# Kernel optimization log

Hardware: AMD Instinct MI355X
Metric: run time of the kernel (lower is better)

The kernel has to match this reference:

```python
import jax, jax.numpy as jnp
import numpy as np

B, A, L, D, IN = 4096, 11, 8, 256, 4
HID = 64  # mlp_dim in MS_HGNN modules
LINE = 64  # line_embedding output dim


def setup_inputs() -> dict:
    key = jax.random.key(0)
    ks = jax.random.split(key, 17)
    s = 0.02
    f = jnp.float32
    return {
        "inputs": jax.random.normal(ks[0], (B * A, L, IN), f),
        "W_in": jax.random.normal(ks[1], (IN, D), f) * s,
        "b_in": jnp.zeros((D,), f),
        "W_pos": jax.random.normal(ks[2], (2 * D, D), f) * s,
        "b_pos": jnp.zeros((D,), f),
        "W_fc2": jax.random.normal(ks[3], (L * D, D), f) * s,
        "b_fc2": jnp.zeros((D,), f),
        "W_fc3": jax.random.normal(ks[4], (D + A, D), f) * s,
        "b_fc3": jnp.zeros((D,), f),
        "Wh1": jax.random.normal(ks[5], (D, HID), f) * s,
        "We1": jax.random.normal(ks[6], (2 * HID, HID), f) * s,
        "Wn1": jax.random.normal(ks[7], (HID, D), f) * s,
        "Wh2": jax.random.normal(ks[8], (D, HID), f) * s,
        "We2": jax.random.normal(ks[9], (2 * HID, HID), f) * s,
        "Wn2": jax.random.normal(ks[10], (HID, D), f) * s,
        "W_line": jax.random.normal(ks[11], (D, LINE), f) * s,
        "batch_size": B,
        "agent_num": A,
    }


def _nmp(xf, Wh, We, Wn, w=None):
    # one round of neural message passing over the (hyper)graph of agents
    h = jax.nn.relu(xf @ Wh)  # [B, A, HID]
    b, a, hd = h.shape
    hi = jnp.broadcast_to(h[:, :, None, :], (b, a, a, hd))
    hj = jnp.broadcast_to(h[:, None, :, :], (b, a, a, hd))
    e = jax.nn.relu(jnp.concatenate([hi, hj], -1) @ We)  # [B, A, A, HID]
    if w is None:
        agg = e.mean(axis=2)
    else:
        agg = (w[..., None] * e).sum(axis=2) / (w.sum(axis=2)[..., None] + 1e-6)
    return agg @ Wn  # [B, A, D]


def reference(inputs, W_in, b_in, W_pos, b_pos, W_fc2, b_fc2, W_fc3, b_fc3,
              Wh1, We1, Wn1, Wh2, We2, Wn2, W_line, batch_size, agent_num):
    d = W_in.shape[1]
    length = inputs.shape[1]
    # input_fc
    tf_in = inputs @ W_in + b_in  # [B*A, L, D]
    # positional encoding (sin/cos interleaved), concat + fc (dropout in eval)
    pos = jnp.arange(length, dtype=tf_in.dtype)[:, None]
    div = jnp.exp(jnp.arange(0, d, 2, dtype=tf_in.dtype) * (-np.log(10000.0) / d))
    ang = pos * div  # [L, D/2]
    pe = jnp.stack([jnp.sin(ang), jnp.cos(ang)], -1).reshape(length, d)
    x = jnp.concatenate([tf_in, jnp.broadcast_to(pe, tf_in.shape)], -1) @ W_pos + b_pos
    # flatten time, input_fc2
    x = x.reshape(batch_size, agent_num, length * d)
    ftraj = x @ W_fc2 + b_fc2  # [B, A, D]
    # add_category (identity one-hot per agent) + input_fc3
    eye = jnp.broadcast_to(jnp.eye(agent_num, dtype=ftraj.dtype),
                           (batch_size, agent_num, agent_num))
    ftraj = jnp.concatenate([ftraj, eye], -1) @ W_fc3 + b_fc3
    # cosine-similarity correlation + per-scene adaptive thresholding
    q = ftraj / jnp.linalg.norm(ftraj, axis=2, keepdims=True)
    corr = jnp.einsum('bad,bcd->bac', q, q)
    a = corr.min(axis=(1, 2), keepdims=True)
    thr = jnp.where(a < 0.4, 0.4,
                    jnp.where((a > 0.4) & (a < 0.6), a + 0.1, a + 0.03))
    corr = jnp.where(corr < thr, jnp.zeros_like(corr), corr)
    adj = (corr > 0).astype(ftraj.dtype)  # binarized dynamic grouping mask
    # ordinary fully-connected interaction
    ftraj_inter = _nmp(ftraj, Wh1, We1, Wn1)
    # group-masked hyper interaction + line embedding
    hyp = _nmp(ftraj, Wh2, We2, Wn2, adj)
    feat_one = hyp @ W_line  # [B, A, LINE]
    out = jnp.concatenate([ftraj, ftraj_inter, feat_one], -1)
    return out.reshape(batch_size * agent_num, -1)
```

## Files before the change

kernel.cpp:

```cpp
#include <hip/hip_runtime.h>

#define TPB 256
#define TPM 192

constexpr int B_ = 4096, A_ = 11;
constexpr int R_ = B_ * A_;

constexpr int M_O     = 0;
constexpr int M2_O    = 8192;
constexpr int WC_O    = 16384;
constexpr int XB_O    = 19712;
constexpr int CB_O    = 21760;
constexpr int B2_O    = 22016;
constexpr int WN2L_O  = 24832;
constexpr int MH1_O   = 28928;
constexpr int BH1_O   = 30976;
constexpr int MH2_O   = 16384;
constexpr int BH2_O   = 18432;


__global__ __launch_bounds__(TPB) void k_preAB(const float* __restrict__ Win,
                                               const float* __restrict__ bin,
                                               const float* __restrict__ Wpos,
                                               const float* __restrict__ bpos,
                                               const float* __restrict__ Wn2,
                                               const float* __restrict__ Wline,
                                               float* __restrict__ ws) {
    __shared__ float red[8 * 33];
    const int t = threadIdx.x, o8 = t & 31, ks = t >> 5;
    const int bx = blockIdx.x;
    if (bx < 32) {
        int o = bx * 32 + o8, i = o >> 8, j = o & 255;
        const float* Ar = Win + i * 256;
        float p = 0.f;
        #pragma unroll 8
        for (int d = ks * 32; d < ks * 32 + 32; ++d) p += Ar[d] * Wpos[d * 256 + j];
        red[ks * 33 + o8] = p;
        __syncthreads();
        if (t < 32) {
            float s = 0.f;
            #pragma unroll
            for (int m = 0; m < 8; ++m) s += red[m * 33 + t];
            ws[WC_O + bx * 32 + t] = s;
        }
    } else if (bx < 96) {
        int o = (bx - 32) * 32 + o8, l = o >> 8, j = o & 255;
        const float c0 = -logf(10000.f) / 256.f;
        float p = 0.f;
        for (int d = ks * 64; d < ks * 64 + 64; ++d) {
            float a;
            if (d < 256) a = bin[d];
            else {
                int dd = d - 256;
                float freq = expf((float)(dd & ~1) * c0);
                float ang = (float)l * freq;
                a = (dd & 1) ? cosf(ang) : sinf(ang);
            }
            p += a * Wpos[d * 256 + j];
        }
        red[ks * 33 + o8] = p;
        __syncthreads();
        if (t < 32) {
            int oo = (bx - 32) * 32 + t;
            float s = bpos[oo & 255];
            #pragma unroll
            for (int m = 0; m < 8; ++m) s += red[m * 33 + t];
            ws[XB_O + oo] = s;
        }
    } else {
        int o = (bx - 96) * 32 + o8, k = o >> 6, c = o & 63;
        const float* Ar = Wn2 + k * 256;
        float p = 0.f;
        #pragma unroll 8
        for (int d = ks * 32; d < ks * 32 + 32; ++d) p += Ar[d] * Wline[d * 64 + c];
        red[ks * 33 + o8] = p;
        __syncthreads();
        if (t < 32) {
            float s = 0.f;
            #pragma unroll
            for (int m = 0; m < 8; ++m) s += red[m * 33 + t];
            ws[WN2L_O + (bx - 96) * 32 + t] = s;
        }
    }
}

__global__ __launch_bounds__(TPB) void k_preC(const float* __restrict__ Wfc2,
                                              const float* __restrict__ bfc2,
                                              float* __restrict__ ws) {
    __shared__ float red[8 * 33];
    const int t = threadIdx.x, o8 = t & 31, ks = t >> 5;
    const int bx = blockIdx.x;
    if (bx < 256) {
        int o = bx * 32 + o8, k = o >> 8, j = o & 255;
        int l = k >> 2, i = k & 3;
        const float* Ar = ws + WC_O + i * 256;
        const float* Br = Wfc2 + l * 65536 + j;
        float p = 0.f;
        #pragma unroll 8
        for (int d = ks * 32; d < ks * 32 + 32; ++d) p += Ar[d] * Br[d * 256];
        red[ks * 33 + o8] = p;
        __syncthreads();
        if (t < 32) {
            float s = 0.f;
            #pragma unroll
            for (int m = 0; m < 8; ++m) s += red[m * 33 + t];
            ws[M_O + bx * 32 + t] = s;
        }
    } else {
        int j = (bx - 256) * 32 + o8;
        const float* Ar = ws + XB_O;
        float p = 0.f;
        #pragma unroll 4
        for (int dk = ks * 256; dk < ks * 256 + 256; ++dk) p += Ar[dk] * Wfc2[dk * 256 + j];
        red[ks * 33 + o8] = p;
        __syncthreads();
        if (t < 32) {
            int jj = (bx - 256) * 32 + t;
            float s = bfc2[jj];
            #pragma unroll
            for (int m = 0; m < 8; ++m) s += red[m * 33 + t];
            ws[CB_O + jj] = s;
        }
    }
}

__global__ __launch_bounds__(TPB) void k_preD(const float* __restrict__ Wfc3,
                                              const float* __restrict__ bfc3,
                                              float* __restrict__ ws) {
    __shared__ float red[8 * 33];
    const int t = threadIdx.x, o8 = t & 31, ks = t >> 5;
    const int bx = blockIdx.x;
    if (bx < 256) {
        int o = bx * 32 + o8, k = o >> 8, j = o & 255;
        const float* Ar = ws + M_O + k * 256;
        float p = 0.f;
        #pragma unroll 8
        for (int d = ks * 32; d < ks * 32 + 32; ++d) p += Ar[d] * Wfc3[d * 256 + j];
        red[ks * 33 + o8] = p;
        __syncthreads();
        if (t < 32) {
            float s = 0.f;
            #pragma unroll
            for (int m = 0; m < 8; ++m) s += red[m * 33 + t];
            ws[M2_O + bx * 32 + t] = s;
        }
    } else {
        int o = (bx - 256) * 32 + o8, j = o & 255;
        const float* Ar = ws + CB_O;
        float p = 0.f;
        #pragma unroll 8
        for (int d = ks * 32; d < ks * 32 + 32; ++d) p += Ar[d] * Wfc3[d * 256 + j];
        red[ks * 33 + o8] = p;
        __syncthreads();
        if (t < 32) {
            int oo = (bx - 256) * 32 + t;
            int aa = oo >> 8, jj = oo & 255;
            float s = bfc3[jj] + Wfc3[(256 + aa) * 256 + jj];
            #pragma unroll
            for (int m = 0; m < 8; ++m) s += red[m * 33 + t];
            ws[B2_O + oo] = s;
        }
    }
}

__global__ __launch_bounds__(TPB) void k_preE(const float* __restrict__ Wh1,
                                              const float* __restrict__ Wh2,
                                              float* __restrict__ ws) {
    __shared__ float red[8 * 33];
    const int t = threadIdx.x, o8 = t & 31, ks = t >> 5;
    const int bx = blockIdx.x;
    const float* Bw;  int oo_base;  int out_o;  int mode;
    if (bx < 64)       { mode = 0; out_o = MH1_O; oo_base = bx * 32;         Bw = Wh1; }
    else if (bx < 86)  { mode = 1; out_o = BH1_O; oo_base = (bx - 64) * 32;  Bw = Wh1; }
    else if (bx < 150) { mode = 0; out_o = MH2_O; oo_base = (bx - 86) * 32;  Bw = Wh2; }
    else               { mode = 1; out_o = BH2_O; oo_base = (bx - 150) * 32; Bw = Wh2; }
    int o = oo_base + o8;
    int r = o >> 6, c = o & 63;
    const float* Aw = ws + (mode == 0 ? M2_O : B2_O) + r * 256;
    float p = 0.f;
    #pragma unroll 8
    for (int d = ks * 32; d < ks * 32 + 32; ++d) p += Aw[d] * Bw[d * 64 + c];
    red[ks * 33 + o8] = p;
    __syncthreads();
    if (t < 32) {
        float s = 0.f;
        #pragma unroll
        for (int m = 0; m < 8; ++m) s += red[m * 33 + t];
        ws[out_o + oo_base + t] = s;
    }
}


__global__ __launch_bounds__(TPM) void k_main(const float* __restrict__ in,
                                              const float* __restrict__ We1g,
                                              const float* __restrict__ We2g,
                                              const float* __restrict__ Wn1,
                                              const float* __restrict__ ws,
                                              float* out) {
    __shared__ float inS[44 * 36];
    __shared__ float bufA[44 * 68];
    __shared__ float bufB[44 * 68];
    __shared__ float Bs[2048];
    __shared__ float dcS[484];
    __shared__ float thrS[4];
    const int t = threadIdx.x;
    const int rg = t >> 4, cg = t & 15;
    const int r0 = rg * 4, c0 = cg * 4;
    const int rowBlk = blockIdx.x * 44;
    const bool act = rg < 11;

    float4 pf0, pf1, pf2;
    auto pfLoad = [&](const float4* lo, const float4* hi) {
        pf0 = lo[t];
        pf1 = (t < 64) ? lo[t + 192] : hi[t - 64];
        if (t < 128) pf2 = hi[t + 128];
    };
    auto pfStore = [&]() {
        float4* d = (float4*)Bs;
        d[t] = pf0; d[t + 192] = pf1;
        if (t < 128) d[t + 384] = pf2;
    };

    pfLoad((const float4*)(ws + M2_O), (const float4*)(ws + M2_O) + 256);
    for (int o = t; o < 352; o += TPM) {
        int row = o >> 3, c4 = o & 7;
        *(float4*)&inS[row * 36 + c4 * 4] =
            *(const float4*)&in[(size_t)(rowBlk + row) * 32 + c4 * 4];
    }
    __syncthreads();

    float acc[4][16];
    #pragma unroll
    for (int r = 0; r < 4; ++r)
        #pragma unroll
        for (int c = 0; c < 16; ++c) acc[r][c] = 0.f;
    for (int kh = 0; kh < 4; ++kh) {
        pfStore();
        if (kh < 3) pfLoad((const float4*)(ws + M2_O) + (kh + 1) * 512,
                           (const float4*)(ws + M2_O) + (kh + 1) * 512 + 256);
        else        pfLoad((const float4*)(ws + MH1_O), (const float4*)(ws + MH1_O) + 256);
        __syncthreads();
        if (act) {
            #pragma unroll
            for (int kq = 0; kq < 2; ++kq) {
                float av[4][4];
                #pragma unroll
                for (int r = 0; r < 4; ++r) {
                    float4 a4 = *(const float4*)&inS[(r0 + r) * 36 + kh * 8 + kq * 4];
                    av[r][0] = a4.x; av[r][1] = a4.y; av[r][2] = a4.z; av[r][3] = a4.w;
                }
                #pragma unroll
                for (int kk = 0; kk < 4; ++kk) {
                    float4 b[4];
                    #pragma unroll
                    for (int j = 0; j < 4; ++j)
                        b[j] = *(const float4*)&Bs[(kq * 4 + kk) * 256 + c0 + j * 64];
                    #pragma unroll
                    for (int r = 0; r < 4; ++r) {
                        float a = av[r][kk];
                        #pragma unroll
                        for (int j = 0; j < 4; ++j) {
                            acc[r][j * 4 + 0] += a * b[j].x;
                            acc[r][j * 4 + 1] += a * b[j].y;
                            acc[r][j * 4 + 2] += a * b[j].z;
                            acc[r][j * 4 + 3] += a * b[j].w;
                        }
                    }
                }
            }
        }
        __syncthreads();
    }
    if (act) {
        #pragma unroll
        for (int r = 0; r < 4; ++r) {
            int row = r0 + r, il = row % 11;
            size_t ob = (size_t)(rowBlk + row) * 576;
            #pragma unroll
            for (int j = 0; j < 4; ++j) {
                float4 b2 = *(const float4*)&ws[B2_O + il * 256 + c0 + j * 64];
                acc[r][j * 4 + 0] += b2.x; acc[r][j * 4 + 1] += b2.y;
                acc[r][j * 4 + 2] += b2.z; acc[r][j * 4 + 3] += b2.w;
                *(float4*)&out[ob + c0 + j * 64] =
                    make_float4(acc[r][j * 4 + 0], acc[r][j * 4 + 1],
                                acc[r][j * 4 + 2], acc[r][j * 4 + 3]);
            }
        }
    }

    bool has0 = false, has1 = false;
    int s0_ = 0, i0_ = 0, j0_ = 0, s1_ = 0, i1_ = 0, j1_ = 0;
    {
        int idx = t;
        if (idx < 264) {
            has0 = true; s0_ = idx / 66; int p = idx % 66; int i = 0;
            while (p >= 11 - i) { p -= 11 - i; ++i; }
            i0_ = i; j0_ = i + p;
        }
        idx = t + TPM;
        if (idx < 264) {
            has1 = true; s1_ = idx / 66; int p = idx % 66; int i = 0;
            while (p >= 11 - i) { p -= 11 - i; ++i; }
            i1_ = i; j1_ = i + p;
        }
    }
    float dacc0 = 0.f, dacc1 = 0.f;
    for (int sl = 0; sl < 4; ++sl) {
        if (act) {
            #pragma unroll
            for (int r = 0; r < 4; ++r)
                *(float4*)&bufA[(r0 + r) * 68 + c0] =
                    make_float4(acc[r][sl * 4 + 0], acc[r][sl * 4 + 1],
                                acc[r][sl * 4 + 2], acc[r][sl * 4 + 3]);
        }
        __syncthreads();
        if (has0) {
            const float* ra = &bufA[(s0_ * 11 + i0_) * 68];
            const float* rb = &bufA[(s0_ * 11 + j0_) * 68];
            #pragma unroll
            for (int c = 0; c < 16; ++c) {
                float4 a = *(const float4*)&ra[c * 4];
                float4 b = *(const float4*)&rb[c * 4];
                dacc0 += a.x * b.x + a.y * b.y + a.z * b.z + a.w * b.w;
            }
        }
        if (has1) {
            const float* ra = &bufA[(s1_ * 11 + i1_) * 68];
            const float* rb = &bufA[(s1_ * 11 + j1_) * 68];
            #pragma unroll
            for (int c = 0; c < 16; ++c) {
                float4 a = *(const float4*)&ra[c * 4];
                float4 b = *(const float4*)&rb[c * 4];
                dacc1 += a.x * b.x + a.y * b.y + a.z * b.z + a.w * b.w;
            }
        }
        __syncthreads();
    }
    if (has0) { dcS[s0_ * 121 + i0_ * 11 + j0_] = dacc0;
                dcS[s0_ * 121 + j0_ * 11 + i0_] = dacc0; }
    if (has1) { dcS[s1_ * 121 + i1_ * 11 + j1_] = dacc1;
                dcS[s1_ * 121 + j1_ * 11 + i1_] = dacc1; }
    __syncthreads();

    {
        float cc0, cc1, cc2 = 0.f;
        {
            int idx = t; int si = idx / 121, p = idx % 121, i = p / 11, j = p % 11;
            cc0 = dcS[idx] * rsqrtf(dcS[si * 121 + i * 12] * dcS[si * 121 + j * 12]);
        }
        {
            int idx = t + TPM; int si = idx / 121, p = idx % 121, i = p / 11, j = p % 11;
            cc1 = dcS[idx] * rsqrtf(dcS[si * 121 + i * 12] * dcS[si * 121 + j * 12]);
        }
        if (t + 2 * TPM < 484) {
            int idx = t + 2 * TPM; int si = idx / 121, p = idx % 121, i = p / 11, j = p % 11;
            cc2 = dcS[idx] * rsqrtf(dcS[si * 121 + i * 12] * dcS[si * 121 + j * 12]);
        }
        __syncthreads();
        dcS[t] = cc0;
        dcS[t + TPM] = cc1;
        if (t + 2 * TPM < 484) dcS[t + 2 * TPM] = cc2;
    }
    __syncthreads();
    if (t < 4) {
        float mn = 3.0e38f;
        for (int p = 0; p < 121; ++p) mn = fminf(mn, dcS[t * 121 + p]);
        thrS[t] = (mn < 0.4f) ? 0.4f : ((mn > 0.4f && mn < 0.6f) ? mn + 0.1f : mn + 0.03f);
    }
    __syncthreads();

    float a1v[4][4];
    for (int st = 0; st < 2; ++st) {
        const float* bh = ws + (st ? BH2_O : BH1_O);
        const float* We = st ? We2g : We1g;
        float* hbuf = st ? bufB : bufA;
        pfStore();
        pfLoad((const float4*)(We), (const float4*)(We + 4096));
        __syncthreads();
        float hh[4][4];
        #pragma unroll
        for (int r = 0; r < 4; ++r)
            #pragma unroll
            for (int c = 0; c < 4; ++c) hh[r][c] = 0.f;
        if (act) {
            #pragma unroll
            for (int kq = 0; kq < 8; ++kq) {
                float av[4][4];
                #pragma unroll
                for (int r = 0; r < 4; ++r) {
                    float4 a4 = *(const float4*)&inS[(r0 + r) * 36 + kq * 4];
                    av[r][0] = a4.x; av[r][1] = a4.y; av[r][2] = a4.z; av[r][3] = a4.w;
                }
                #pragma unroll
                for (int kk = 0; kk < 4; ++kk) {
                    float4 b = *(const float4*)&Bs[(kq * 4 + kk) * 64 + c0];
                    #pragma unroll
                    for (int r = 0; r < 4; ++r) {
                        float a = av[r][kk];
                        hh[r][0] += a * b.x; hh[r][1] += a * b.y;
                        hh[r][2] += a * b.z; hh[r][3] += a * b.w;
                    }
                }
            }
            #pragma unroll
            for (int r = 0; r < 4; ++r) {
                int il = (r0 + r) % 11;
                float4 b = *(const float4*)&bh[il * 64 + c0];
                *(float4*)&hbuf[(r0 + r) * 68 + c0] =
                    make_float4(fmaxf(hh[r][0] + b.x, 0.f), fmaxf(hh[r][1] + b.y, 0.f),
                                fmaxf(hh[r][2] + b.z, 0.f), fmaxf(hh[r][3] + b.w, 0.f));
            }
        }
        __syncthreads();
        float uu[4][4], vv[4][4];
        #pragma unroll
        for (int r = 0; r < 4; ++r)
            #pragma unroll
            for (int c = 0; c < 4; ++c) { uu[r][c] = 0.f; vv[r][c] = 0.f; }
        for (int kh = 0; kh < 4; ++kh) {
            pfStore();
            if (kh < 3)
                pfLoad((const float4*)(We + (kh + 1) * 1024),
                       (const float4*)(We + 4096 + (kh + 1) * 1024));
            else if (st == 0)
                pfLoad((const float4*)(ws + MH2_O), (const float4*)(ws + MH2_O) + 256);
            else
                pfLoad((const float4*)(Wn1), (const float4*)(Wn1) + 256);
            __syncthreads();
            if (act) {
                #pragma unroll
                for (int kq = 0; kq < 4; ++kq) {
                    float av[4][4];
                    #pragma unroll
                    for (int r = 0; r < 4; ++r) {
                        float4 a4 = *(const float4*)&hbuf[(r0 + r) * 68 + kh * 16 + kq * 4];
                        av[r][0] = a4.x; av[r][1] = a4.y; av[r][2] = a4.z; av[r][3] = a4.w;
                    }
                    #pragma unroll
                    for (int kk = 0; kk < 4; ++kk) {
                        float4 bu = *(const float4*)&Bs[(kq * 4 + kk) * 64 + c0];
                        float4 bv = *(const float4*)&Bs[1024 + (kq * 4 + kk) * 64 + c0];
                        #pragma unroll
                        for (int r = 0; r < 4; ++r) {
                            float a = av[r][kk];
                            uu[r][0] += a * bu.x; uu[r][1] += a * bu.y;
                            uu[r][2] += a * bu.z; uu[r][3] += a * bu.w;
                            vv[r][0] += a * bv.x; vv[r][1] += a * bv.y;
                            vv[r][2] += a * bv.z; vv[r][3] += a * bv.w;
                        }
                    }
                }
            }
            __syncthreads();
        }
        if (act) {
            #pragma unroll
            for (int r = 0; r < 4; ++r)
                *(float4*)&bufB[(r0 + r) * 68 + c0] =
                    make_float4(vv[r][0], vv[r][1], vv[r][2], vv[r][3]);
        }
        __syncthreads();
        if (act) {
            #pragma unroll
            for (int r = 0; r < 4; ++r) {
                int row = r0 + r, s = row / 11, il = row - s * 11;
                float th = thrS[s];
                float t0 = 0.f, t1 = 0.f, t2 = 0.f, t3 = 0.f, cnt = 0.f;
                #pragma unroll
                for (int j = 0; j < 11; ++j) {
                    float4 vj = *(const float4*)&bufB[(s * 11 + j) * 68 + c0];
                    if (st == 0) {
                        t0 += fmaxf(uu[r][0] + vj.x, 0.f);
                        t1 += fmaxf(uu[r][1] + vj.y, 0.f);
                        t2 += fmaxf(uu[r][2] + vj.z, 0.f);
                        t3 += fmaxf(uu[r][3] + vj.w, 0.f);
                    } else {
                        float adj = (dcS[s * 121 + il * 11 + j] >= th) ? 1.f : 0.f;
                        t0 += adj * fmaxf(uu[r][0] + vj.x, 0.f);
                        t1 += adj * fmaxf(uu[r][1] + vj.y, 0.f);
                        t2 += adj * fmaxf(uu[r][2] + vj.z, 0.f);
                        t3 += adj * fmaxf(uu[r][3] + vj.w, 0.f);
                        cnt += adj;
                    }
                }
                float inv = (st == 0) ? (1.f / 11.f) : (1.f / (cnt + 1e-6f));
                a1v[r][0] = t0 * inv; a1v[r][1] = t1 * inv;
                a1v[r][2] = t2 * inv; a1v[r][3] = t3 * inv;
            }
        }
        __syncthreads();
        if (act) {
            float* dst = st ? bufB : bufA;
            #pragma unroll
            for (int r = 0; r < 4; ++r)
                *(float4*)&dst[(r0 + r) * 68 + c0] =
                    make_float4(a1v[r][0], a1v[r][1], a1v[r][2], a1v[r][3]);
        }
        __syncthreads();
    }

    {
        float ac2[4][16];
        #pragma unroll
        for (int r = 0; r < 4; ++r)
            #pragma unroll
            for (int c = 0; c < 16; ++c) ac2[r][c] = 0.f;
        for (int kh = 0; kh < 8; ++kh) {
            pfStore();
            if (kh < 7) pfLoad((const float4*)(Wn1) + (kh + 1) * 512,
                               (const float4*)(Wn1) + (kh + 1) * 512 + 256);
            else        pfLoad((const float4*)(ws + WN2L_O), (const float4*)(ws + WN2L_O) + 256);
            __syncthreads();
            if (act) {
                #pragma unroll
                for (int kq = 0; kq < 2; ++kq) {
                    float av[4][4];
                    #pragma unroll
                    for (int r = 0; r < 4; ++r) {
                        float4 a4 = *(const float4*)&bufA[(r0 + r) * 68 + kh * 8 + kq * 4];
                        av[r][0] = a4.x; av[r][1] = a4.y; av[r][2] = a4.z; av[r][3] = a4.w;
                    }
                    #pragma unroll
                    for (int kk = 0; kk < 4; ++kk) {
                        float4 b[4];
                        #pragma unroll
                        for (int j = 0; j < 4; ++j)
                            b[j] = *(const float4*)&Bs[(kq * 4 + kk) * 256 + c0 + j * 64];
                        #pragma unroll
                        for (int r = 0; r < 4; ++r) {
                            float a = av[r][kk];
                            #pragma unroll
                            for (int j = 0; j < 4; ++j) {
                                ac2[r][j * 4 + 0] += a * b[j].x;
                                ac2[r][j * 4 + 1] += a * b[j].y;
                                ac2[r][j * 4 + 2] += a * b[j].z;
                                ac2[r][j * 4 + 3] += a * b[j].w;
                            }
                        }
                    }
                }
            }
            __syncthreads();
        }
        if (act) {
            #pragma unroll
            for (int r = 0; r < 4; ++r) {
                size_t ob = (size_t)(rowBlk + r0 + r) * 576 + 256;
                #pragma unroll
                for (int j = 0; j < 4; ++j)
                    *(float4*)&out[ob + c0 + j * 64] =
                        make_float4(ac2[r][j * 4 + 0], ac2[r][j * 4 + 1],
                                    ac2[r][j * 4 + 2], ac2[r][j * 4 + 3]);
            }
        }
    }

    {
        float fa[4][4];
        #pragma unroll
        for (int r = 0; r < 4; ++r)
            #pragma unroll
            for (int c = 0; c < 4; ++c) fa[r][c] = 0.f;
        for (int kh = 0; kh < 2; ++kh) {
            pfStore();
            if (kh == 0) pfLoad((const float4*)(ws + WN2L_O) + 512,
                                (const float4*)(ws + WN2L_O) + 768);
            __syncthreads();
            if (act) {
                #pragma unroll
                for (int kq = 0; kq < 8; ++kq) {
                    float av[4][4];
                    #pragma unroll
                    for (int r = 0; r < 4; ++r) {
                        float4 a4 = *(const float4*)&bufB[(r0 + r) * 68 + kh * 32 + kq * 4];
                        av[r][0] = a4.x; av[r][1] = a4.y; av[r][2] = a4.z; av[r][3] = a4.w;
                    }
                    #pragma unroll
                    for (int kk = 0; kk < 4; ++kk) {
                        float4 b = *(const float4*)&Bs[(kq * 4 + kk) * 64 + c0];
                        #pragma unroll
                        for (int r = 0; r < 4; ++r) {
                            float a = av[r][kk];
                            fa[r][0] += a * b.x; fa[r][1] += a * b.y;
                            fa[r][2] += a * b.z; fa[r][3] += a * b.w;
                        }
                    }
                }
            }
            __syncthreads();
        }
        if (act) {
            #pragma unroll
            for (int r = 0; r < 4; ++r)
                *(float4*)&out[(size_t)(rowBlk + r0 + r) * 576 + 512 + c0] =
                    make_float4(fa[r][0], fa[r][1], fa[r][2], fa[r][3]);
        }
    }
}

extern "C" void kernel_launch(void* const* d_in, const int* in_sizes, int n_in,
                              void* d_out, int out_size, void* d_ws, size_t ws_size,
                              hipStream_t stream) {
    (void)in_sizes; (void)n_in; (void)out_size; (void)ws_size;
    const float* in     = (const float*)d_in[0];
    const float* W_in   = (const float*)d_in[1];
    const float* b_in   = (const float*)d_in[2];
    const float* W_pos  = (const float*)d_in[3];
    const float* b_pos  = (const float*)d_in[4];
    const float* W_fc2  = (const float*)d_in[5];
    const float* b_fc2  = (const float*)d_in[6];
    const float* W_fc3  = (const float*)d_in[7];
    const float* b_fc3  = (const float*)d_in[8];
    const float* Wh1    = (const float*)d_in[9];
    const float* We1    = (const float*)d_in[10];
    const float* Wn1    = (const float*)d_in[11];
    const float* Wh2    = (const float*)d_in[12];
    const float* We2    = (const float*)d_in[13];
    const float* Wn2    = (const float*)d_in[14];
    const float* W_line = (const float*)d_in[15];
    float* out = (float*)d_out;
    float* ws  = (float*)d_ws;

    k_preAB<<<224, TPB, 0, stream>>>(W_in, b_in, W_pos, b_pos, Wn2, W_line, ws);
    k_preC<<<264, TPB, 0, stream>>>(W_fc2, b_fc2, ws);
    k_preD<<<344, TPB, 0, stream>>>(W_fc3, b_fc3, ws);
    k_preE<<<172, TPB, 0, stream>>>(Wh1, Wh2, ws);
    k_main<<<1024, TPM, 0, stream>>>(in, We1, We2, Wn1, ws, out);
}
```

Before: 168.1 us.

## Split final Wn1/Wline projections into separate tail kernel and merge weight-prep kernels

```diff
diff --git a/kernel.cpp b/kernel.cpp
--- a/kernel.cpp
+++ b/kernel.cpp
@@ -9,44 +9,45 @@
 constexpr int M_O     = 0;
 constexpr int M2_O    = 8192;
 constexpr int WC_O    = 16384;
-constexpr int XB_O    = 19712;
-constexpr int CB_O    = 21760;
-constexpr int B2_O    = 22016;
-constexpr int WN2L_O  = 24832;
-constexpr int MH1_O   = 28928;
-constexpr int BH1_O   = 30976;
-constexpr int MH2_O   = 16384;
-constexpr int BH2_O   = 18432;
-
-
-__global__ __launch_bounds__(TPB) void k_preAB(const float* __restrict__ Win,
-                                               const float* __restrict__ bin,
-                                               const float* __restrict__ Wpos,
-                                               const float* __restrict__ bpos,
-                                               const float* __restrict__ Wn2,
-                                               const float* __restrict__ Wline,
-                                               float* __restrict__ ws) {
+constexpr int XB_O    = 17408;
+constexpr int CB_O    = 19456;
+constexpr int B2_O    = 19712;
+constexpr int WN2L_O  = 22528;
+constexpr int MH1_O   = 26624;
+constexpr int BH1_O   = 28672;
+constexpr int MH2_O   = 29376;
+constexpr int BH2_O   = 31424;
+constexpr int WFA1_O  = 32768;
+constexpr int WFA2_O  = 49152;
+constexpr int BEYE1_O = 65536;
+constexpr int BEYE2_O = 66240;
+constexpr int BB1_O   = 66944;
+constexpr int BB2_O   = 67008;
+constexpr int AG1_O   = 67584;
+constexpr int SZ_RH   = R_ * 64;
+constexpr int AG2_O   = AG1_O + SZ_RH;
+
+
+__global__ __launch_bounds__(TPB) void k_preA(const float* __restrict__ Win,
+                                              const float* __restrict__ bin,
+                                              const float* __restrict__ Wpos,
+                                              const float* __restrict__ bpos,
+                                              const float* __restrict__ Wn2,
+                                              const float* __restrict__ Wline,
+                                              const float* __restrict__ Wfc3,
+                                              const float* __restrict__ bfc3,
+                                              const float* __restrict__ Wh1,
+                                              const float* __restrict__ Wh2,
+                                              float* __restrict__ ws) {
     __shared__ float red[8 * 33];
     const int t = threadIdx.x, o8 = t & 31, ks = t >> 5;
     const int bx = blockIdx.x;
-    if (bx < 32) {
-        int o = bx * 32 + o8, i = o >> 8, j = o & 255;
-        const float* Ar = Win + i * 256;
-        float p = 0.f;
-        #pragma unroll 8
-        for (int d = ks * 32; d < ks * 32 + 32; ++d) p += Ar[d] * Wpos[d * 256 + j];
-        red[ks * 33 + o8] = p;
-        __syncthreads();
-        if (t < 32) {
-            float s = 0.f;
-            #pragma unroll
-            for (int m = 0; m < 8; ++m) s += red[m * 33 + t];
-            ws[WC_O + bx * 32 + t] = s;
-        }
-    } else if (bx < 96) {
-        int o = (bx - 32) * 32 + o8, l = o >> 8, j = o & 255;
+    float p = 0.f;
+    float base_add = 0.f;
+    int out_idx = -1;
+    if (bx < 64) {
+        int o = bx * 32 + o8, l = o >> 8, j = o & 255;
         const float c0 = -logf(10000.f) / 256.f;
-        float p = 0.f;
         for (int d = ks * 64; d < ks * 64 + 64; ++d) {
             float a;
             if (d < 256) a = bin[d];
@@ -58,29 +59,57 @@
             }
             p += a * Wpos[d * 256 + j];
         }
-        red[ks * 33 + o8] = p;
-        __syncthreads();
-        if (t < 32) {
-            int oo = (bx - 32) * 32 + t;
-            float s = bpos[oo & 255];
-            #pragma unroll
-            for (int m = 0; m < 8; ++m) s += red[m * 33 + t];
-            ws[XB_O + oo] = s;
-        }
+        out_idx = XB_O + o; base_add = bpos[j];
+    } else if (bx < 192) {
+        int o = (bx - 64) * 32 + o8, k = o >> 6, c = o & 63;
+        #pragma unroll 8
+        for (int d = ks * 32; d < ks * 32 + 32; ++d) p += Wn2[k * 256 + d] * Wline[d * 64 + c];
+        out_idx = WN2L_O + o;
+    } else if (bx < 704) {
+        int o = (bx - 192) * 32 + o8, e = o >> 6, c = o & 63;
+        #pragma unroll 8
+        for (int d = ks * 32; d < ks * 32 + 32; ++d) p += Wfc3[e * 256 + d] * Wh1[d * 64 + c];
+        out_idx = WFA1_O + o;
+    } else if (bx < 1216) {
+        int o = (bx - 704) * 32 + o8, e = o >> 6, c = o & 63;
+        #pragma unroll 8
+        for (int d = ks * 32; d < ks * 32 + 32; ++d) p += Wfc3[e * 256 + d] * Wh2[d * 64 + c];
+        out_idx = WFA2_O + o;
+    } else if (bx < 1238) {
+        int o = (bx - 1216) * 32 + o8, a = o >> 6, c = o & 63;
+        #pragma unroll 8
+        for (int d = ks * 32; d < ks * 32 + 32; ++d) p += Wfc3[(256 + a) * 256 + d] * Wh1[d * 64 + c];
+        out_idx = BEYE1_O + o;
+    } else if (bx < 1260) {
+        int o = (bx - 1238) * 32 + o8, a = o >> 6, c = o & 63;
+        #pragma unroll 8
+        for (int d = ks * 32; d < ks * 32 + 32; ++d) p += Wfc3[(256 + a) * 256 + d] * Wh2[d * 64 + c];
+        out_idx = BEYE2_O + o;
+    } else if (bx < 1262) {
+        int c = (bx - 1260) * 32 + o8;
+        #pragma unroll 8
+        for (int d = ks * 32; d < ks * 32 + 32; ++d) p += bfc3[d] * Wh1[d * 64 + c];
+        out_idx = BB1_O + c;
+    } else if (bx < 1264) {
+        int c = (bx - 1262) * 32 + o8;
+        #pragma unroll 8
+        for (int d = ks * 32; d < ks * 32 + 32; ++d) p += bfc3[d] * Wh2[d * 64 + c];
+        out_idx = BB2_O + c;
     } else {
-        int o = (bx - 96) * 32 + o8, k = o >> 6, c = o & 63;
-        const float* Ar = Wn2 + k * 256;
-        float p = 0.f;
-        #pragma unroll 8
-        for (int d = ks * 32; d < ks * 32 + 32; ++d) p += Ar[d] * Wline[d * 64 + c];
-        red[ks * 33 + o8] = p;
-        __syncthreads();
-        if (t < 32) {
-            float s = 0.f;
-            #pragma unroll
-            for (int m = 0; m < 8; ++m) s += red[m * 33 + t];
-            ws[WN2L_O + (bx - 96) * 32 + t] = s;
-        }
+        int o = (bx - 1264) * 32 + o8, i = o >> 8, j = o & 255;
+        #pragma unroll 8
+        for (int d = ks * 32; d < ks * 32 + 32; ++d) p += Win[i * 256 + d] * Wpos[d * 256 + j];
+        out_idx = WC_O + o;
+    }
+    red[ks * 33 + o8] = p;
+    __shared__ float baseS[32];
+    if (ks == 0) baseS[o8] = base_add;
+    __syncthreads();
+    if (t < 32) {
+        float s = baseS[t];
+        #pragma unroll
+        for (int m = 0; m < 8; ++m) s += red[m * 33 + t];
+        ws[out_idx - o8 + t] = s;
     }
 }
 
@@ -130,76 +159,81 @@
     __shared__ float red[8 * 33];
     const int t = threadIdx.x, o8 = t & 31, ks = t >> 5;
     const int bx = blockIdx.x;
+    float p = 0.f;
+    int out_base = -1;
+    float fin = 0.f;
+    int oo32 = 0;
     if (bx < 256) {
         int o = bx * 32 + o8, k = o >> 8, j = o & 255;
         const float* Ar = ws + M_O + k * 256;
-        float p = 0.f;
         #pragma unroll 8
         for (int d = ks * 32; d < ks * 32 + 32; ++d) p += Ar[d] * Wfc3[d * 256 + j];
-        red[ks * 33 + o8] = p;
-        __syncthreads();
-        if (t < 32) {
-            float s = 0.f;
-            #pragma unroll
-            for (int m = 0; m < 8; ++m) s += red[m * 33 + t];
-            ws[M2_O + bx * 32 + t] = s;
-        }
-    } else {
+        out_base = M2_O; oo32 = bx * 32;
+    } else if (bx < 344) {
         int o = (bx - 256) * 32 + o8, j = o & 255;
         const float* Ar = ws + CB_O;
-        float p = 0.f;
         #pragma unroll 8
         for (int d = ks * 32; d < ks * 32 + 32; ++d) p += Ar[d] * Wfc3[d * 256 + j];
-        red[ks * 33 + o8] = p;
-        __syncthreads();
-        if (t < 32) {
-            int oo = (bx - 256) * 32 + t;
+        out_base = B2_O; oo32 = (bx - 256) * 32;
+    } else if (bx < 408) {
+        int o = (bx - 344) * 32 + o8, k = o >> 6, c = o & 63;
+        const float* Ar = ws + M_O + k * 256;
+        const float* Br = ws + WFA1_O;
+        #pragma unroll 8
+        for (int d = ks * 32; d < ks * 32 + 32; ++d) p += Ar[d] * Br[d * 64 + c];
+        out_base = MH1_O; oo32 = (bx - 344) * 32;
+    } else if (bx < 472) {
+        int o = (bx - 408) * 32 + o8, k = o >> 6, c = o & 63;
+        const float* Ar = ws + M_O + k * 256;
+        const float* Br = ws + WFA2_O;
+        #pragma unroll 8
+        for (int d = ks * 32; d < ks * 32 + 32; ++d) p += Ar[d] * Br[d * 64 + c];
+        out_base = MH2_O; oo32 = (bx - 408) * 32;
+    } else if (bx < 494) {
+        int o = (bx - 472) * 32 + o8, c = o & 63;
+        const float* Ar = ws + CB_O;
+        const float* Br = ws + WFA1_O;
+        #pragma unroll 8
+        for (int d = ks * 32; d < ks * 32 + 32; ++d) p += Ar[d] * Br[d * 64 + c];
+        out_base = BH1_O; oo32 = (bx - 472) * 32;
+    } else {
+        int o = (bx - 494) * 32 + o8, c = o & 63;
+        const float* Ar = ws + CB_O;
+        const float* Br = ws + WFA2_O;
+        #pragma unroll 8
+        for (int d = ks * 32; d < ks * 32 + 32; ++d) p += Ar[d] * Br[d * 64 + c];
+        out_base = BH2_O; oo32 = (bx - 494) * 32;
+    }
+    red[ks * 33 + o8] = p;
+    __syncthreads();
+    if (t < 32) {
+        int oo = oo32 + t;
+        float s;
+        if (out_base == B2_O) {
             int aa = oo >> 8, jj = oo & 255;
-            float s = bfc3[jj] + Wfc3[(256 + aa) * 256 + jj];
-            #pragma unroll
-            for (int m = 0; m < 8; ++m) s += red[m * 33 + t];
-            ws[B2_O + oo] = s;
-        }
-    }
-}
-
-__global__ __launch_bounds__(TPB) void k_preE(const float* __restrict__ Wh1,
-                                              const float* __restrict__ Wh2,
-                                              float* __restrict__ ws) {
-    __shared__ float red[8 * 33];
-    const int t = threadIdx.x, o8 = t & 31, ks = t >> 5;
-    const int bx = blockIdx.x;
-    const float* Bw;  int oo_base;  int out_o;  int mode;
-    if (bx < 64)       { mode = 0; out_o = MH1_O; oo_base = bx * 32;         Bw = Wh1; }
-    else if (bx < 86)  { mode = 1; out_o = BH1_O; oo_base = (bx - 64) * 32;  Bw = Wh1; }
-    else if (bx < 150) { mode = 0; out_o = MH2_O; oo_base = (bx - 86) * 32;  Bw = Wh2; }
-    else               { mode = 1; out_o = BH2_O; oo_base = (bx - 150) * 32; Bw = Wh2; }
-    int o = oo_base + o8;
-    int r = o >> 6, c = o & 63;
-    const float* Aw = ws + (mode == 0 ? M2_O : B2_O) + r * 256;
-    float p = 0.f;
-    #pragma unroll 8
-    for (int d = ks * 32; d < ks * 32 + 32; ++d) p += Aw[d] * Bw[d * 64 + c];
-    red[ks * 33 + o8] = p;
-    __syncthreads();
-    if (t < 32) {
-        float s = 0.f;
+            s = bfc3[jj] + Wfc3[(256 + aa) * 256 + jj];
+        } else if (out_base == BH1_O) {
+            int aa = oo >> 6, cc = oo & 63;
+            s = ws[BB1_O + cc] + ws[BEYE1_O + aa * 64 + cc];
+        } else if (out_base == BH2_O) {
+            int aa = oo >> 6, cc = oo & 63;
+            s = ws[BB2_O + cc] + ws[BEYE2_O + aa * 64 + cc];
+        } else s = 0.f;
         #pragma unroll
         for (int m = 0; m < 8; ++m) s += red[m * 33 + t];
-        ws[out_o + oo_base + t] = s;
-    }
+        ws[out_base + oo] = s;
+    }
+    (void)fin;
 }
 
 
 __global__ __launch_bounds__(TPM) void k_main(const float* __restrict__ in,
                                               const float* __restrict__ We1g,
                                               const float* __restrict__ We2g,
-                                              const float* __restrict__ Wn1,
-                                              const float* __restrict__ ws,
+                                              float* ws,
                                               float* out) {
     __shared__ float inS[44 * 36];
-    __shared__ float bufA[44 * 68];
-    __shared__ float bufB[44 * 68];
+    __shared__ float buf[44 * 68];
     __shared__ float Bs[2048];
     __shared__ float dcS[484];
     __shared__ float thrS[4];
@@ -309,14 +343,14 @@
         if (act) {
             #pragma unroll
             for (int r = 0; r < 4; ++r)
-                *(float4*)&bufA[(r0 + r) * 68 + c0] =
+                *(float4*)&buf[(r0 + r) * 68 + c0] =
                     make_float4(acc[r][sl * 4 + 0], acc[r][sl * 4 + 1],
                                 acc[r][sl * 4 + 2], acc[r][sl * 4 + 3]);
         }
         __syncthreads();
         if (has0) {
-            const float* ra = &bufA[(s0_ * 11 + i0_) * 68];
-            const float* rb = &bufA[(s0_ * 11 + j0_) * 68];
+            const float* ra = &buf[(s0_ * 11 + i0_) * 68];
+            const float* rb = &buf[(s0_ * 11 + j0_) * 68];
             #pragma unroll
             for (int c = 0; c < 16; ++c) {
                 float4 a = *(const float4*)&ra[c * 4];
@@ -325,8 +359,8 @@
             }
         }
         if (has1) {
-            const float* ra = &bufA[(s1_ * 11 + i1_) * 68];
-            const float* rb = &bufA[(s1_ * 11 + j1_) * 68];
+            const float* ra = &buf[(s1_ * 11 + i1_) * 68];
+            const float* rb = &buf[(s1_ * 11 + j1_) * 68];
             #pragma unroll
             for (int c = 0; c < 16; ++c) {
                 float4 a = *(const float4*)&ra[c * 4];
@@ -369,11 +403,9 @@
     }
     __syncthreads();
 
-    float a1v[4][4];
     for (int st = 0; st < 2; ++st) {
         const float* bh = ws + (st ? BH2_O : BH1_O);
         const float* We = st ? We2g : We1g;
-        float* hbuf = st ? bufB : bufA;
         pfStore();
         pfLoad((const float4*)(We), (const float4*)(We + 4096));
         __syncthreads();
@@ -406,7 +438,7 @@
             for (int r = 0; r < 4; ++r) {
                 int il = (r0 + r) % 11;
                 float4 b = *(const float4*)&bh[il * 64 + c0];
-                *(float4*)&hbuf[(r0 + r) * 68 + c0] =
+                *(float4*)&buf[(r0 + r) * 68 + c0] =
                     make_float4(fmaxf(hh[r][0] + b.x, 0.f), fmaxf(hh[r][1] + b.y, 0.f),
                                 fmaxf(hh[r][2] + b.z, 0.f), fmaxf(hh[r][3] + b.w, 0.f));
             }
@@ -424,8 +456,6 @@
                        (const float4*)(We + 4096 + (kh + 1) * 1024));
             else if (st == 0)
                 pfLoad((const float4*)(ws + MH2_O), (const float4*)(ws + MH2_O) + 256);
-            else
-                pfLoad((const float4*)(Wn1), (const float4*)(Wn1) + 256);
             __syncthreads();
             if (act) {
                 #pragma unroll
@@ -433,7 +463,7 @@
                     float av[4][4];
                     #pragma unroll
                     for (int r = 0; r < 4; ++r) {
-                        float4 a4 = *(const float4*)&hbuf[(r0 + r) * 68 + kh * 16 + kq * 4];
+                        float4 a4 = *(const float4*)&buf[(r0 + r) * 68 + kh * 16 + kq * 4];
                         av[r][0] = a4.x; av[r][1] = a4.y; av[r][2] = a4.z; av[r][3] = a4.w;
                     }
                     #pragma unroll
@@ -456,11 +486,12 @@
         if (act) {
             #pragma unroll
             for (int r = 0; r < 4; ++r)
-                *(float4*)&bufB[(r0 + r) * 68 + c0] =
+                *(float4*)&buf[(r0 + r) * 68 + c0] =
                     make_float4(vv[r][0], vv[r][1], vv[r][2], vv[r][3]);
         }
         __syncthreads();
         if (act) {
+            float* ag = ws + (st ? AG2_O : AG1_O);
             #pragma unroll
             for (int r = 0; r < 4; ++r) {
                 int row = r0 + r, s = row / 11, il = row - s * 11;
@@ -468,7 +499,7 @@
                 float t0 = 0.f, t1 = 0.f, t2 = 0.f, t3 = 0.f, cnt = 0.f;
                 #pragma unroll
                 for (int j = 0; j < 11; ++j) {
-                    float4 vj = *(const float4*)&bufB[(s * 11 + j) * 68 + c0];
+                    float4 vj = *(const float4*)&buf[(s * 11 + j) * 68 + c0];
                     if (st == 0) {
                         t0 += fmaxf(uu[r][0] + vj.x, 0.f);
                         t1 += fmaxf(uu[r][1] + vj.y, 0.f);
@@ -484,77 +515,98 @@
                     }
                 }
                 float inv = (st == 0) ? (1.f / 11.f) : (1.f / (cnt + 1e-6f));
-                a1v[r][0] = t0 * inv; a1v[r][1] = t1 * inv;
-                a1v[r][2] = t2 * inv; a1v[r][3] = t3 * inv;
-            }
-        }
-        __syncthreads();
-        if (act) {
-            float* dst = st ? bufB : bufA;
-            #pragma unroll
-            for (int r = 0; r < 4; ++r)
-                *(float4*)&dst[(r0 + r) * 68 + c0] =
-                    make_float4(a1v[r][0], a1v[r][1], a1v[r][2], a1v[r][3]);
-        }
-        __syncthreads();
-    }
+                *(float4*)&ag[(size_t)(rowBlk + row) * 64 + c0] =
+                    make_float4(t0 * inv, t1 * inv, t2 * inv, t3 * inv);
+            }
+        }
+        __syncthreads();
+    }
+}
+
+
+__global__ __launch_bounds__(TPB) void k_tail(const float* __restrict__ Wn1,
+                                              const float* __restrict__ ws,
+                                              float* __restrict__ out) {
+    __shared__ float aS[64 * 68];
+    __shared__ float Bs[2048];
+    const int t = threadIdx.x;
+    const int rowBase = blockIdx.x * 64;
+    const int tg = t >> 4, tc = t & 15;
+    const int r0 = tg * 4, c0 = tc * 4;
 
     {
-        float ac2[4][16];
+        const float4* s1 = (const float4*)(ws + AG1_O + (size_t)rowBase * 64);
+        #pragma unroll
+        for (int o = t; o < 1024; o += TPB) {
+            int row = o >> 4, c4 = o & 15;
+            *(float4*)&aS[row * 68 + c4 * 4] = s1[o];
+        }
+    }
+    __syncthreads();
+
+    {
+        float acc[4][16];
         #pragma unroll
         for (int r = 0; r < 4; ++r)
             #pragma unroll
-            for (int c = 0; c < 16; ++c) ac2[r][c] = 0.f;
+            for (int c = 0; c < 16; ++c) acc[r][c] = 0.f;
         for (int kh = 0; kh < 8; ++kh) {
-            pfStore();
-            if (kh < 7) pfLoad((const float4*)(Wn1) + (kh + 1) * 512,
-                               (const float4*)(Wn1) + (kh + 1) * 512 + 256);
-            else        pfLoad((const float4*)(ws + WN2L_O), (const float4*)(ws + WN2L_O) + 256);
+            if (kh) __syncthreads();
+            {
+                const float4* src = (const float4*)(Wn1 + kh * 2048);
+                float4* dst = (float4*)Bs;
+                dst[t] = src[t];
+                dst[t + 256] = src[t + 256];
+            }
             __syncthreads();
-            if (act) {
-                #pragma unroll
-                for (int kq = 0; kq < 2; ++kq) {
-                    float av[4][4];
+            #pragma unroll
+            for (int kq = 0; kq < 2; ++kq) {
+                float av[4][4];
+                #pragma unroll
+                for (int r = 0; r < 4; ++r) {
+                    float4 a4 = *(const float4*)&aS[(r0 + r) * 68 + kh * 8 + kq * 4];
+                    av[r][0] = a4.x; av[r][1] = a4.y; av[r][2] = a4.z; av[r][3] = a4.w;
+                }
+                #pragma unroll
+                for (int kk = 0; kk < 4; ++kk) {
+                    float4 b[4];
+                    #pragma unroll
+                    for (int j = 0; j < 4; ++j)
+                        b[j] = *(const float4*)&Bs[(kq * 4 + kk) * 256 + c0 + j * 64];
                     #pragma unroll
                     for (int r = 0; r < 4; ++r) {
-                        float4 a4 = *(const float4*)&bufA[(r0 + r) * 68 + kh * 8 + kq * 4];
-                        av[r][0] = a4.x; av[r][1] = a4.y; av[r][2] = a4.z; av[r][3] = a4.w;
-                    }
-                    #pragma unroll
-                    for (int kk = 0; kk < 4; ++kk) {
-                        float4 b[4];
+                        float a = av[r][kk];
                         #pragma unroll
-                        for (int j = 0; j < 4; ++j)
-                            b[j] = *(const float4*)&Bs[(kq * 4 + kk) * 256 + c0 + j * 64];
-                        #pragma unroll
-                        for (int r = 0; r < 4; ++r) {
-                            float a = av[r][kk];
-                            #pragma unroll
-                            for (int j = 0; j < 4; ++j) {
-                                ac2[r][j * 4 + 0] += a * b[j].x;
-                                ac2[r][j * 4 + 1] += a * b[j].y;
-                                ac2[r][j * 4 + 2] += a * b[j].z;
-                                ac2[r][j * 4 + 3] += a * b[j].w;
-                            }
+                        for (int j = 0; j < 4; ++j) {
+                            acc[r][j * 4 + 0] += a * b[j].x;
+                            acc[r][j * 4 + 1] += a * b[j].y;
+                            acc[r][j * 4 + 2] += a * b[j].z;
+                            acc[r][j * 4 + 3] += a * b[j].w;
                         }
                     }
                 }
             }
-            __syncthreads();
-        }
-        if (act) {
-            #pragma unroll
-            for (int r = 0; r < 4; ++r) {
-                size_t ob = (size_t)(rowBlk + r0 + r) * 576 + 256;
-                #pragma unroll
-                for (int j = 0; j < 4; ++j)
-                    *(float4*)&out[ob + c0 + j * 64] =
-                        make_float4(ac2[r][j * 4 + 0], ac2[r][j * 4 + 1],
-                                    ac2[r][j * 4 + 2], ac2[r][j * 4 + 3]);
-            }
-        }
-    }
-
+        }
+        #pragma unroll
+        for (int r = 0; r < 4; ++r) {
+            size_t ob = (size_t)(rowBase + r0 + r) * 576 + 256;
+            #pragma unroll
+            for (int j = 0; j < 4; ++j)
+                *(float4*)&out[ob + c0 + j * 64] =
+                    make_float4(acc[r][j * 4 + 0], acc[r][j * 4 + 1],
+                                acc[r][j * 4 + 2], acc[r][j * 4 + 3]);
+        }
+    }
+
+    __syncthreads();
+    {
+        const float4* s2 = (const float4*)(ws + AG2_O + (size_t)rowBase * 64);
+        #pragma unroll
+        for (int o = t; o < 1024; o += TPB) {
+            int row = o >> 4, c4 = o & 15;
+            *(float4*)&aS[row * 68 + c4 * 4] = s2[o];
+        }
+    }
     {
         float fa[4][4];
         #pragma unroll
@@ -562,39 +614,38 @@
             #pragma unroll
             for (int c = 0; c < 4; ++c) fa[r][c] = 0.f;
         for (int kh = 0; kh < 2; ++kh) {
-            pfStore();
-            if (kh == 0) pfLoad((const float4*)(ws + WN2L_O) + 512,
-                                (const float4*)(ws + WN2L_O) + 768);
             __syncthreads();
-            if (act) {
-                #pragma unroll
-                for (int kq = 0; kq < 8; ++kq) {
-                    float av[4][4];
+            {
+                const float4* src = (const float4*)(ws + WN2L_O + kh * 2048);
+                float4* dst = (float4*)Bs;
+                dst[t] = src[t];
+                dst[t + 256] = src[t + 256];
+            }
+            __syncthreads();
+            #pragma unroll
+            for (int kq = 0; kq < 8; ++kq) {
+                float av[4][4];
+                #pragma unroll
+                for (int r = 0; r < 4; ++r) {
+                    float4 a4 = *(const float4*)&aS[(r0 + r) * 68 + kh * 32 + kq * 4];
+                    av[r][0] = a4.x; av[r][1] = a4.y; av[r][2] = a4.z; av[r][3] = a4.w;
+                }
+                #pragma unroll
+                for (int kk = 0; kk < 4; ++kk) {
+                    float4 b = *(const float4*)&Bs[(kq * 4 + kk) * 64 + c0];
                     #pragma unroll
                     for (int r = 0; r < 4; ++r) {
-                        float4 a4 = *(const float4*)&bufB[(r0 + r) * 68 + kh * 32 + kq * 4];
-                        av[r][0] = a4.x; av[r][1] = a4.y; av[r][2] = a4.z; av[r][3] = a4.w;
+                        float a = av[r][kk];
+                        fa[r][0] += a * b.x; fa[r][1] += a * b.y;
+                        fa[r][2] += a * b.z; fa[r][3] += a * b.w;
                     }
-                    #pragma unroll
-                    for (int kk = 0; kk < 4; ++kk) {
-                        float4 b = *(const float4*)&Bs[(kq * 4 + kk) * 64 + c0];
-                        #pragma unroll
-                        for (int r = 0; r < 4; ++r) {
-                            float a = av[r][kk];
-                            fa[r][0] += a * b.x; fa[r][1] += a * b.y;
-                            fa[r][2] += a * b.z; fa[r][3] += a * b.w;
-                        }
-                    }
-                }
-            }
-            __syncthreads();
-        }
-        if (act) {
-            #pragma unroll
-            for (int r = 0; r < 4; ++r)
-                *(float4*)&out[(size_t)(rowBlk + r0 + r) * 576 + 512 + c0] =
-                    make_float4(fa[r][0], fa[r][1], fa[r][2], fa[r][3]);
-        }
+                }
+            }
+        }
+        #pragma unroll
+        for (int r = 0; r < 4; ++r)
+            *(float4*)&out[(size_t)(rowBase + r0 + r) * 576 + 512 + c0] =
+                make_float4(fa[r][0], fa[r][1], fa[r][2], fa[r][3]);
     }
 }
 
@@ -621,9 +672,10 @@
     float* out = (float*)d_out;
     float* ws  = (float*)d_ws;
 
-    k_preAB<<<224, TPB, 0, stream>>>(W_in, b_in, W_pos, b_pos, Wn2, W_line, ws);
+    k_preA<<<1296, TPB, 0, stream>>>(W_in, b_in, W_pos, b_pos, Wn2, W_line,
+                                     W_fc3, b_fc3, Wh1, Wh2, ws);
     k_preC<<<264, TPB, 0, stream>>>(W_fc2, b_fc2, ws);
-    k_preD<<<344, TPB, 0, stream>>>(W_fc3, b_fc3, ws);
-    k_preE<<<172, TPB, 0, stream>>>(Wh1, Wh2, ws);
-    k_main<<<1024, TPM, 0, stream>>>(in, We1, We2, Wn1, ws, out);
+    k_preD<<<516, TPB, 0, stream>>>(W_fc3, b_fc3, ws);
+    k_main<<<1024, TPM, 0, stream>>>(in, We1, We2, ws, out);
+    k_tail<<<R_ / 64, TPB, 0, stream>>>(Wn1, ws, out);
 }
```

Result: faster. 163.5 us (-2.8%).
